# Optimization experiments

Measured on AMD Instinct MI355X. Metric: run time of the kernel, lower is better.

The kernel has to match this reference:

```python
import jax, jax.numpy as jnp
import numpy as np
import math

H, HD = 16, 64
EPS = 1e-6


def setup_inputs() -> dict:
    key = jax.random.key(0)
    ks = jax.random.split(key, 6)
    B, T, D = 4, 2048, 1024
    s = 0.02
    return {
        "x": jax.random.normal(ks[0], (B, T, D), jnp.float32),
        "wq": jax.random.normal(ks[1], (D, D), jnp.float32) * s,
        "wk": jax.random.normal(ks[2], (D, D), jnp.float32) * s,
        "wv": jax.random.normal(ks[3], (D, D), jnp.float32) * s,
        "wo": jax.random.normal(ks[4], (D, D), jnp.float32) * s,
        "norm_g": jnp.ones((D,), jnp.float32),
    }


def reference(x, wq, wk, wv, wo, norm_g):
    B, T, D = x.shape
    scale = math.sqrt(HD)
    # nn.Linear(D, D, bias=False): y = x @ W.T
    q = (x @ wq.T).reshape(B, T, H, HD).transpose(0, 2, 1, 3)  # [B,H,T,HD]
    k = (x @ wk.T).reshape(B, T, H, HD).transpose(0, 2, 1, 3)
    v = (x @ wv.T).reshape(B, T, H, HD).transpose(0, 2, 1, 3)
    scores = jnp.einsum("bhqd,bhkd->bhqk", q, k) / scale  # [B,H,T,T]
    causal = jnp.tril(jnp.ones((T, T), bool))  # True where allowed
    scores = jnp.where(causal, scores, -jnp.inf)
    attn = jax.nn.softmax(scores, axis=-1)  # dropout p=0 -> identity
    out = jnp.einsum("bhqk,bhkd->bhqd", attn, v)  # [B,H,T,HD]
    out = out.transpose(0, 2, 1, 3).reshape(B, T, D)
    y = x + out @ wo.T  # residual
    # RMSNorm
    rms = jnp.sqrt(jnp.mean(y * y, axis=-1, keepdims=True) + EPS)
    return (y / rms) * norm_g
```

## Files before the change

kernel.cpp:

```cpp
#include <hip/hip_runtime.h>
#include <hip/hip_bf16.h>

constexpr int NB  = 4;
constexpr int NT  = 2048;
constexpr int ND  = 1024;
constexpr int NH  = 16;
constexpr int NHD = 64;
constexpr int NM  = NB * NT;

typedef unsigned short u16;
typedef __attribute__((ext_vector_type(8))) short  short8;
typedef __attribute__((ext_vector_type(4))) float  f32x4;

__device__ __forceinline__ u16 f2bf(float f) {
  unsigned u = __builtin_bit_cast(unsigned, f);
  u += 0x7FFFu + ((u >> 16) & 1u);
  return (u16)(u >> 16);
}

__device__ __forceinline__ unsigned pk2bf(float lo, float hi_) {
  float2 t; t.x = lo; t.y = hi_;
  __hip_bfloat162 h2 = __float22bfloat162_rn(t);
  unsigned u;
  __builtin_memcpy(&u, &h2, 4);
  return u;
}

__device__ __forceinline__ void gll16(const u16* src, u16* dst) {
  __builtin_amdgcn_global_load_lds(
      (const __attribute__((address_space(1))) void*)src,
      (__attribute__((address_space(3))) void*)dst, 16, 0, 0);
}

__global__ __launch_bounds__(256) void cast_all(
    const float* __restrict__ x,
    const float* __restrict__ w0, const float* __restrict__ w1,
    const float* __restrict__ w2, const float* __restrict__ w3,
    u16* __restrict__ xb,
    u16* __restrict__ o0, u16* __restrict__ o1,
    u16* __restrict__ o2, u16* __restrict__ o3) {
  const int bid = blockIdx.x;
  const float* in;
  u16* out;
  int i;
  if (bid < 8192) {
    in = x; out = xb; i = bid * 256 + threadIdx.x;
  } else {
    const int z = (bid - 8192) >> 10;
    in  = (z == 0) ? w0 : (z == 1) ? w1 : (z == 2) ? w2 : w3;
    out = (z == 0) ? o0 : (z == 1) ? o1 : (z == 2) ? o2 : o3;
    i = ((bid - 8192) & 1023) * 256 + threadIdx.x;
  }
  float4 v = ((const float4*)in)[i];
  ushort4 o;
  o.x = f2bf(v.x); o.y = f2bf(v.y); o.z = f2bf(v.z); o.w = f2bf(v.w);
  ((ushort4*)out)[i] = o;
}

__global__ __launch_bounds__(512, 2) void gemm_qkvm(
    const u16* __restrict__ xb,
    const u16* __restrict__ wqb, const u16* __restrict__ wkb, const u16* __restrict__ wvb,
    u16* __restrict__ Qb, u16* __restrict__ Kb, u16* __restrict__ VTb) {
  const int row0 = blockIdx.x << 7;
  const int col0 = blockIdx.y << 7;
  const float scl = 0.125f * 1.44269504f;

  const int tid  = threadIdx.x;
  const int lane = tid & 63, wid = tid >> 6;
  const int wm = wid >> 2, wn = wid & 3;
  const int li = lane & 15, hi = lane >> 4;
  const int l3 = lane >> 3, sl = lane & 7;
  const int schunk = ((sl ^ l3) << 3);

  extern __shared__ __align__(16) u16 smem[];
  u16* lA = smem;
  u16* lB = smem + 2 * 128 * 64;

  auto stage = [&](int t) {
    const int bf = t & 1;
    const int k0 = t << 6;
#pragma unroll
    for (int h = 0; h < 2; ++h) {
      int r = h * 64 + wid * 8;
      size_t go = (size_t)(col0 + r + l3) * ND + k0 + schunk;
      gll16(&xb [(size_t)(row0 + r + l3) * ND + k0 + schunk], &lA[bf * 8192 + r * 64]);
      gll16(&wqb[go], &lB[(bf * 3 + 0) * 8192 + r * 64]);
      gll16(&wkb[go], &lB[(bf * 3 + 1) * 8192 + r * 64]);
      gll16(&wvb[go], &lB[(bf * 3 + 2) * 8192 + r * 64]);
    }
  };

  f32x4 acc[3][4][2] = {};

  stage(0);
  asm volatile("s_waitcnt vmcnt(0)" ::: "memory");
  __builtin_amdgcn_s_barrier();

  for (int i = 0; i < 16; ++i) {
    if (i + 1 < 16) stage(i + 1);

    const u16* la = &lA[(i & 1) * 8192];

    short8 a[4][2];
#pragma unroll
    for (int m = 0; m < 4; ++m)
#pragma unroll
      for (int c = 0; c < 2; ++c)
        a[m][c] = *(const short8*)&la[(wm * 64 + m * 16 + li) * 64 + (((c * 4 + hi) ^ (li & 7)) << 3)];

#pragma unroll
    for (int z = 0; z < 3; ++z) {
      const u16* lb = &lB[((i & 1) * 3 + z) * 8192];
      short8 b[2][2];
#pragma unroll
      for (int n = 0; n < 2; ++n)
#pragma unroll
        for (int c = 0; c < 2; ++c)
          b[n][c] = *(const short8*)&lb[(wn * 32 + n * 16 + li) * 64 + (((c * 4 + hi) ^ (li & 7)) << 3)];

      if (z == 2) {
#pragma unroll
        for (int m = 0; m < 4; ++m)
#pragma unroll
          for (int n = 0; n < 2; ++n)
#pragma unroll
            for (int c = 0; c < 2; ++c)
              acc[z][m][n] = __builtin_amdgcn_mfma_f32_16x16x32_bf16(a[m][c], b[n][c], acc[z][m][n], 0, 0, 0);
      } else {
#pragma unroll
        for (int m = 0; m < 4; ++m)
#pragma unroll
          for (int n = 0; n < 2; ++n)
#pragma unroll
            for (int c = 0; c < 2; ++c)
              acc[z][m][n] = __builtin_amdgcn_mfma_f32_16x16x32_bf16(b[n][c], a[m][c], acc[z][m][n], 0, 0, 0);
      }
    }

    if (i + 1 < 16) { asm volatile("s_waitcnt vmcnt(0)" ::: "memory"); }
    __builtin_amdgcn_s_barrier();
  }

#pragma unroll
  for (int m = 0; m < 4; ++m)
#pragma unroll
    for (int n = 0; n < 2; ++n) {
      {
        int token = row0 + wm * 64 + m * 16 + li;
        int feat0 = col0 + wn * 32 + n * 16 + hi * 4;
        int b_ = token >> 11, t_ = token & (NT - 1);
        int h_ = feat0 >> 6,  d0 = feat0 & (NHD - 1);
        uint2 w;
        w.x = pk2bf(acc[0][m][n][0] * scl, acc[0][m][n][1] * scl);
        w.y = pk2bf(acc[0][m][n][2] * scl, acc[0][m][n][3] * scl);
        *(uint2*)&Qb[(((size_t)(b_ * NH + h_)) * NT + t_) * NHD + d0] = w;
      }
      {
        int token = row0 + wm * 64 + m * 16 + li;
        int feat0 = col0 + wn * 32 + n * 16 + hi * 4;
        int b_ = token >> 11, t_ = token & (NT - 1);
        int h_ = feat0 >> 6,  d0 = feat0 & (NHD - 1);
        uint2 w;
        w.x = pk2bf(acc[1][m][n][0], acc[1][m][n][1]);
        w.y = pk2bf(acc[1][m][n][2], acc[1][m][n][3]);
        *(uint2*)&Kb[(((size_t)(b_ * NH + h_)) * NT + t_) * NHD + d0] = w;
      }
      {
        int token0 = row0 + wm * 64 + m * 16 + hi * 4;
        int col    = col0 + wn * 32 + n * 16 + li;
        int b_ = token0 >> 11, t0 = token0 & (NT - 1);
        int h_ = col >> 6,     d_ = col & (NHD - 1);
        uint2 w;
        w.x = pk2bf(acc[2][m][n][0], acc[2][m][n][1]);
        w.y = pk2bf(acc[2][m][n][2], acc[2][m][n][3]);
        *(uint2*)&VTb[(((size_t)(b_ * NH + h_)) * NHD + d_) * NT + t0] = w;
      }
    }
}

__global__ __launch_bounds__(512, 2) void gemm_wo3(
    const u16* __restrict__ ao, const u16* __restrict__ wob,
    const float* __restrict__ x, float* __restrict__ y) {
  const int row0 = blockIdx.x << 7;
  const int col0 = blockIdx.y << 7;

  const int tid  = threadIdx.x;
  const int lane = tid & 63, wid = tid >> 6;
  const int wm = wid >> 2, wn = wid & 3;
  const int li = lane & 15, hi = lane >> 4;
  const int l3 = lane >> 3, sl = lane & 7;
  const int schunk = ((sl ^ l3) << 3);

  extern __shared__ __align__(16) u16 smem[];
  u16* lAb = smem;
  u16* lBb = smem + 3 * 128 * 64;

  auto stage = [&](int t) {
    const int bo = (t % 3) * 8192;
    const int k0 = t << 6;
#pragma unroll
    for (int h = 0; h < 2; ++h) {
      int r = h * 64 + wid * 8;
      gll16(&ao [(size_t)(row0 + r + l3) * ND + k0 + schunk], &lAb[bo + r * 64]);
      gll16(&wob[(size_t)(col0 + r + l3) * ND + k0 + schunk], &lBb[bo + r * 64]);
    }
  };

  f32x4 acc[4][2] = {};

  stage(0);
  stage(1);

  for (int i = 0; i < 16; ++i) {
    if (i < 15) { asm volatile("s_waitcnt vmcnt(4)" ::: "memory"); }
    else        { asm volatile("s_waitcnt vmcnt(0)" ::: "memory"); }
    __builtin_amdgcn_s_barrier();

    if (i + 2 < 16) stage(i + 2);

    const u16* la = &lAb[(i % 3) * 8192];
    const u16* lb = &lBb[(i % 3) * 8192];

    short8 a[4][2], b[2][2];
#pragma unroll
    for (int m = 0; m < 4; ++m)
#pragma unroll
      for (int c = 0; c < 2; ++c)
        a[m][c] = *(const short8*)&la[(wm * 64 + m * 16 + li) * 64 + (((c * 4 + hi) ^ (li & 7)) << 3)];
#pragma unroll
    for (int n = 0; n < 2; ++n)
#pragma unroll
      for (int c = 0; c < 2; ++c)
        b[n][c] = *(const short8*)&lb[(wn * 32 + n * 16 + li) * 64 + (((c * 4 + hi) ^ (li & 7)) << 3)];

#pragma unroll
    for (int m = 0; m < 4; ++m)
#pragma unroll
      for (int n = 0; n < 2; ++n)
#pragma unroll
        for (int c = 0; c < 2; ++c)
          acc[m][n] = __builtin_amdgcn_mfma_f32_16x16x32_bf16(b[n][c], a[m][c], acc[m][n], 0, 0, 0);
  }

#pragma unroll
  for (int m = 0; m < 4; ++m)
#pragma unroll
    for (int n = 0; n < 2; ++n) {
      int token = row0 + wm * 64 + m * 16 + li;
      int feat0 = col0 + wn * 32 + n * 16 + hi * 4;
      size_t idx = (size_t)token * ND + feat0;
      float4 xv = *(const float4*)&x[idx];
      float4 o;
      o.x = acc[m][n][0] + xv.x; o.y = acc[m][n][1] + xv.y;
      o.z = acc[m][n][2] + xv.z; o.w = acc[m][n][3] + xv.w;
      *(float4*)&y[idx] = o;
    }
}

__global__ __launch_bounds__(256) void attn_kernel(
    const u16* __restrict__ Q, const u16* __restrict__ K, const u16* __restrict__ VT,
    u16* __restrict__ AO) {
  const int nb  = gridDim.x * gridDim.y;
  const int b0  = blockIdx.y * gridDim.x + blockIdx.x;
  const int L   = (b0 & 7) * (nb >> 3) + (b0 >> 3);
  const int qb  = 31 - (L & 31);
  const int bh  = L >> 5;

  const int tid = threadIdx.x;
  const int lane = tid & 63, wid = tid >> 6;
  const int li = lane & 15, hi = lane >> 4;
  const int r0 = qb * 64 + wid * 16;
  const int qrow = r0 + li;
  const size_t bK = (size_t)bh * NT * NHD;
  const size_t bV = (size_t)bh * NHD * NT;

  __shared__ __align__(16) u16 lK [2][64 * 64];
  __shared__ __align__(16) u16 lVT[3][64 * 64];
  __shared__ __align__(16) u16 lP [4][16 * 64];

  const int ch0 = tid, ch1 = tid + 256;
  const int d0 = (ch0 >> 3) * 64 + (((ch0 & 7) ^ ((ch0 >> 3) & 7)) << 3);
  const int d1 = (ch1 >> 3) * 64 + (((ch1 & 7) ^ ((ch1 >> 3) & 7)) << 3);
  const int vOff0 = (ch0 >> 3) * NT + (ch0 & 7) * 8;
  const int vOff1 = (ch1 >> 3) * NT + (ch1 & 7) * 8;

  uint4 gK0, gK1, gV0, gV1;
  auto issue = [&](int kt) {
    const u16* kp = K + bK + (size_t)kt * 4096;
    const u16* vp = VT + bV + kt * 64;
    gK0 = *(const uint4*)&kp[ch0 * 8];
    gK1 = *(const uint4*)&kp[ch1 * 8];
    gV0 = *(const uint4*)&vp[vOff0];
    gV1 = *(const uint4*)&vp[vOff1];
  };
  auto commit = [&](int kt) {
    *(uint4*)&lK [kt & 1][d0] = gK0;
    *(uint4*)&lK [kt & 1][d1] = gK1;
    *(uint4*)&lVT[kt % 3][d0] = gV0;
    *(uint4*)&lVT[kt % 3][d1] = gV1;
  };

  short8 qf[2];
#pragma unroll
  for (int c = 0; c < 2; ++c)
    qf[c] = *(const short8*)&Q[bK + (size_t)qrow * NHD + c * 32 + hi * 8];

  short8 vone;
#pragma unroll
  for (int e = 0; e < 8; ++e) vone[e] = (short)0x3F80;

  f32x4 o[4] = {};
  f32x4 o4 = {};
  short8 pap0, pap1;

  issue(0);
  commit(0);
  __syncthreads();

  const int pswz = (li & 7) << 1;

  for (int kt = 0; kt <= qb; ++kt) {
    if (kt < qb) issue(kt + 1);

    f32x4 s[4] = {};
    __builtin_amdgcn_s_setprio(1);
#pragma unroll
    for (int g = 0; g < 4; ++g)
#pragma unroll
      for (int c = 0; c < 2; ++c) {
        short8 kf = *(const short8*)&lK[kt & 1][(g * 16 + li) * 64 + ((c * 4 + hi) ^ (li & 7)) * 8];
        s[g] = __builtin_amdgcn_mfma_f32_16x16x32_bf16(kf, qf[c], s[g], 0, 0, 0);
      }

    if (kt > 0) {
      const u16* lv = lVT[(kt - 1) % 3];
#pragma unroll
      for (int gd = 0; gd < 4; ++gd) {
        short8 vf0 = *(const short8*)&lv[(gd * 16 + li) * 64 + ((0 * 4 + hi) ^ (li & 7)) * 8];
        short8 vf1 = *(const short8*)&lv[(gd * 16 + li) * 64 + ((1 * 4 + hi) ^ (li & 7)) * 8];
        o[gd] = __builtin_amdgcn_mfma_f32_16x16x32_bf16(vf0, pap0, o[gd], 0, 0, 0);
        o[gd] = __builtin_amdgcn_mfma_f32_16x16x32_bf16(vf1, pap1, o[gd], 0, 0, 0);
      }
      o4 = __builtin_amdgcn_mfma_f32_16x16x32_bf16(vone, pap0, o4, 0, 0, 0);
      o4 = __builtin_amdgcn_mfma_f32_16x16x32_bf16(vone, pap1, o4, 0, 0, 0);
    }
    __builtin_amdgcn_s_setprio(0);

    if (kt == qb) {
#pragma unroll
      for (int g = 0; g < 4; ++g)
#pragma unroll
        for (int rg = 0; rg < 4; ++rg) {
          int kcol = kt * 64 + g * 16 + hi * 4 + rg;
          if (kcol > qrow) s[g][rg] = -INFINITY;
        }
    }

#pragma unroll
    for (int g = 0; g < 4; ++g) {
      float p0 = __builtin_amdgcn_exp2f(s[g][0]);
      float p1 = __builtin_amdgcn_exp2f(s[g][1]);
      float p2 = __builtin_amdgcn_exp2f(s[g][2]);
      float p3 = __builtin_amdgcn_exp2f(s[g][3]);
      uint2 w;
      w.x = pk2bf(p0, p1);
      w.y = pk2bf(p2, p3);
      int k8s = (g * 4 + hi) ^ pswz;
      *(uint2*)&lP[wid][li * 64 + k8s * 4] = w;
    }

    pap0 = *(const short8*)&lP[wid][li * 64 + ((0 * 8 + hi * 2) ^ pswz) * 4];
    pap1 = *(const short8*)&lP[wid][li * 64 + ((1 * 8 + hi * 2) ^ pswz) * 4];

    if (kt < qb) commit(kt + 1);
    __syncthreads();
  }

  {
    const u16* lv = lVT[qb % 3];
#pragma unroll
    for (int gd = 0; gd < 4; ++gd) {
      short8 vf0 = *(const short8*)&lv[(gd * 16 + li) * 64 + ((0 * 4 + hi) ^ (li & 7)) * 8];
      short8 vf1 = *(const short8*)&lv[(gd * 16 + li) * 64 + ((1 * 4 + hi) ^ (li & 7)) * 8];
      o[gd] = __builtin_amdgcn_mfma_f32_16x16x32_bf16(vf0, pap0, o[gd], 0, 0, 0);
      o[gd] = __builtin_amdgcn_mfma_f32_16x16x32_bf16(vf1, pap1, o[gd], 0, 0, 0);
    }
    o4 = __builtin_amdgcn_mfma_f32_16x16x32_bf16(vone, pap0, o4, 0, 0, 0);
    o4 = __builtin_amdgcn_mfma_f32_16x16x32_bf16(vone, pap1, o4, 0, 0, 0);
  }

  const int b_ = bh >> 4, h_ = bh & 15;
  const float inv = 1.0f / o4[0];
  const size_t rowbase = ((size_t)(b_ * NT + qrow)) * ND + h_ * 64;
#pragma unroll
  for (int gd = 0; gd < 4; ++gd) {
    uint2 w;
    w.x = pk2bf(o[gd][0] * inv, o[gd][1] * inv);
    w.y = pk2bf(o[gd][2] * inv, o[gd][3] * inv);
    *(uint2*)&AO[rowbase + gd * 16 + hi * 4] = w;
  }
}

__global__ __launch_bounds__(256) void rmsnorm_kernel(float* __restrict__ y,
                                                      const float* __restrict__ g) {
  const int row = blockIdx.x;
  const int tid = threadIdx.x;
  const int lane = tid & 63, wid = tid >> 6;
  float4 v = ((const float4*)(y + (size_t)row * ND))[tid];
  float ss = v.x * v.x + v.y * v.y + v.z * v.z + v.w * v.w;
#pragma unroll
  for (int off = 32; off; off >>= 1) ss += __shfl_down(ss, off);
  __shared__ float red[4];
  if (lane == 0) red[wid] = ss;
  __syncthreads();
  float tot = red[0] + red[1] + red[2] + red[3];
  float inv = rsqrtf(tot * (1.0f / (float)ND) + 1e-6f);
  float4 gg = ((const float4*)g)[tid];
  float4 o;
  o.x = v.x * inv * gg.x; o.y = v.y * inv * gg.y;
  o.z = v.z * inv * gg.z; o.w = v.w * inv * gg.w;
  ((float4*)(y + (size_t)row * ND))[tid] = o;
}

extern "C" void kernel_launch(void* const* d_in, const int* in_sizes, int n_in,
                              void* d_out, int out_size, void* d_ws, size_t ws_size,
                              hipStream_t stream) {
  const float* x  = (const float*)d_in[0];
  const float* wq = (const float*)d_in[1];
  const float* wk = (const float*)d_in[2];
  const float* wv = (const float*)d_in[3];
  const float* wo = (const float*)d_in[4];
  const float* ng = (const float*)d_in[5];
  float* out = (float*)d_out;

  char* ws = (char*)d_ws;
  u16* xb  = (u16*)(ws);
  u16* wqb = (u16*)(ws + (16u << 20));
  u16* wkb = (u16*)(ws + (18u << 20));
  u16* wvb = (u16*)(ws + (20u << 20));
  u16* wob = (u16*)(ws + (22u << 20));
  u16* Qb  = (u16*)(ws + (24u << 20));
  u16* Kb  = (u16*)(ws + (40u << 20));
  u16* VTb = (u16*)(ws + (56u << 20));
  u16* AO  = (u16*)(ws + (72u << 20));

  cast_all<<<8192 + 4096, 256, 0, stream>>>(x, wq, wk, wv, wo, xb, wqb, wkb, wvb, wob);

  gemm_qkvm<<<dim3(64, 8), 512, 131072, stream>>>(xb, wqb, wkb, wvb, Qb, Kb, VTb);
  attn_kernel<<<dim3(NT / 64, NB * NH), 256, 0, stream>>>(Qb, Kb, VTb, AO);
  gemm_wo3<<<dim3(64, 8), 512, 98304, stream>>>(AO, wob, x, out);
  rmsnorm_kernel<<<NM, 256, 0, stream>>>(out, ng);
}
```

Before: 183.5 us.

## Process two KV tiles per iteration with four-deep K/V LDS buffers

Restructures the causal attention loop so each iteration loads, scores, softmaxes and accumulates two 64-wide KV tiles, with K and V staged in four LDS slots. This halves the number of block barriers and global load rounds, and removes the skewed PV-from-previous-tile pipeline in favour of in-iteration PV right after each tile's exponentials. In exchange, LDS grows from about 48KB to 72KB per block and register pressure rises, which can reduce blocks per CU. The old overlap of PV MFMAs with the next tile's QK is lost. When qb is even, the extra prefetched tile is loaded but never used.

```diff
diff --git a/kernel.cpp b/kernel.cpp
--- a/kernel.cpp
+++ b/kernel.cpp
@@ -274,8 +274,8 @@
   const size_t bK = (size_t)bh * NT * NHD;
   const size_t bV = (size_t)bh * NHD * NT;
 
-  __shared__ __align__(16) u16 lK [2][64 * 64];
-  __shared__ __align__(16) u16 lVT[3][64 * 64];
+  __shared__ __align__(16) u16 lK [4][64 * 64];
+  __shared__ __align__(16) u16 lVT[4][64 * 64];
   __shared__ __align__(16) u16 lP [4][16 * 64];
 
   const int ch0 = tid, ch1 = tid + 256;
@@ -284,20 +284,32 @@
   const int vOff0 = (ch0 >> 3) * NT + (ch0 & 7) * 8;
   const int vOff1 = (ch1 >> 3) * NT + (ch1 & 7) * 8;
 
-  uint4 gK0, gK1, gV0, gV1;
-  auto issue = [&](int kt) {
-    const u16* kp = K + bK + (size_t)kt * 4096;
-    const u16* vp = VT + bV + kt * 64;
-    gK0 = *(const uint4*)&kp[ch0 * 8];
-    gK1 = *(const uint4*)&kp[ch1 * 8];
-    gV0 = *(const uint4*)&vp[vOff0];
-    gV1 = *(const uint4*)&vp[vOff1];
+  uint4 gKa0, gKa1, gVa0, gVa1;
+  uint4 gKb0, gKb1, gVb0, gVb1;
+  auto issue = [&](int j) {
+    const u16* kpa = K + bK + (size_t)(2 * j) * 4096;
+    const u16* vpa = VT + bV + (size_t)(2 * j) * 64;
+    gKa0 = *(const uint4*)&kpa[ch0 * 8];
+    gKa1 = *(const uint4*)&kpa[ch1 * 8];
+    gVa0 = *(const uint4*)&vpa[vOff0];
+    gVa1 = *(const uint4*)&vpa[vOff1];
+    const u16* kpb = kpa + 4096;
+    const u16* vpb = vpa + 64;
+    gKb0 = *(const uint4*)&kpb[ch0 * 8];
+    gKb1 = *(const uint4*)&kpb[ch1 * 8];
+    gVb0 = *(const uint4*)&vpb[vOff0];
+    gVb1 = *(const uint4*)&vpb[vOff1];
   };
-  auto commit = [&](int kt) {
-    *(uint4*)&lK [kt & 1][d0] = gK0;
-    *(uint4*)&lK [kt & 1][d1] = gK1;
-    *(uint4*)&lVT[kt % 3][d0] = gV0;
-    *(uint4*)&lVT[kt % 3][d1] = gV1;
+  auto commit = [&](int j) {
+    const int ba = (2 * j) & 3, bb = (2 * j + 1) & 3;
+    *(uint4*)&lK [ba][d0] = gKa0;
+    *(uint4*)&lK [ba][d1] = gKa1;
+    *(uint4*)&lVT[ba][d0] = gVa0;
+    *(uint4*)&lVT[ba][d1] = gVa1;
+    *(uint4*)&lK [bb][d0] = gKb0;
+    *(uint4*)&lK [bb][d1] = gKb1;
+    *(uint4*)&lVT[bb][d0] = gVb0;
+    *(uint4*)&lVT[bb][d1] = gVb1;
   };
 
   short8 qf[2];
@@ -311,82 +323,121 @@
 
   f32x4 o[4] = {};
   f32x4 o4 = {};
-  short8 pap0, pap1;
 
   issue(0);
   commit(0);
   __syncthreads();
 
+  const int jmax = qb >> 1;
   const int pswz = (li & 7) << 1;
 
-  for (int kt = 0; kt <= qb; ++kt) {
-    if (kt < qb) issue(kt + 1);
-
-    f32x4 s[4] = {};
+  for (int j = 0; j <= jmax; ++j) {
+    if (j < jmax) issue(j + 1);
+
+    const int s0t = 2 * j, s1t = 2 * j + 1;
+    const bool act1 = (s1t <= qb);
+
+    f32x4 sA[4] = {}, sB[4] = {};
     __builtin_amdgcn_s_setprio(1);
 #pragma unroll
     for (int g = 0; g < 4; ++g)
 #pragma unroll
       for (int c = 0; c < 2; ++c) {
-        short8 kf = *(const short8*)&lK[kt & 1][(g * 16 + li) * 64 + ((c * 4 + hi) ^ (li & 7)) * 8];
-        s[g] = __builtin_amdgcn_mfma_f32_16x16x32_bf16(kf, qf[c], s[g], 0, 0, 0);
-      }
-
-    if (kt > 0) {
-      const u16* lv = lVT[(kt - 1) % 3];
+        short8 kf = *(const short8*)&lK[s0t & 3][(g * 16 + li) * 64 + ((c * 4 + hi) ^ (li & 7)) * 8];
+        sA[g] = __builtin_amdgcn_mfma_f32_16x16x32_bf16(kf, qf[c], sA[g], 0, 0, 0);
+      }
+    if (act1) {
+#pragma unroll
+      for (int g = 0; g < 4; ++g)
+#pragma unroll
+        for (int c = 0; c < 2; ++c) {
+          short8 kf = *(const short8*)&lK[s1t & 3][(g * 16 + li) * 64 + ((c * 4 + hi) ^ (li & 7)) * 8];
+          sB[g] = __builtin_amdgcn_mfma_f32_16x16x32_bf16(kf, qf[c], sB[g], 0, 0, 0);
+        }
+    }
+    __builtin_amdgcn_s_setprio(0);
+
+    if (s0t == qb) {
+#pragma unroll
+      for (int g = 0; g < 4; ++g)
+#pragma unroll
+        for (int rg = 0; rg < 4; ++rg) {
+          int kcol = s0t * 64 + g * 16 + hi * 4 + rg;
+          if (kcol > qrow) sA[g][rg] = -INFINITY;
+        }
+    }
+    if (act1 && s1t == qb) {
+#pragma unroll
+      for (int g = 0; g < 4; ++g)
+#pragma unroll
+        for (int rg = 0; rg < 4; ++rg) {
+          int kcol = s1t * 64 + g * 16 + hi * 4 + rg;
+          if (kcol > qrow) sB[g][rg] = -INFINITY;
+        }
+    }
+
+    {
+#pragma unroll
+      for (int g = 0; g < 4; ++g) {
+        float p0 = __builtin_amdgcn_exp2f(sA[g][0]);
+        float p1 = __builtin_amdgcn_exp2f(sA[g][1]);
+        float p2 = __builtin_amdgcn_exp2f(sA[g][2]);
+        float p3 = __builtin_amdgcn_exp2f(sA[g][3]);
+        uint2 w;
+        w.x = pk2bf(p0, p1);
+        w.y = pk2bf(p2, p3);
+        int k8s = (g * 4 + hi) ^ pswz;
+        *(uint2*)&lP[wid][li * 64 + k8s * 4] = w;
+      }
+      short8 pa0 = *(const short8*)&lP[wid][li * 64 + ((0 * 8 + hi * 2) ^ pswz) * 4];
+      short8 pa1 = *(const short8*)&lP[wid][li * 64 + ((1 * 8 + hi * 2) ^ pswz) * 4];
+
+      const u16* lv = lVT[s0t & 3];
+      __builtin_amdgcn_s_setprio(1);
 #pragma unroll
       for (int gd = 0; gd < 4; ++gd) {
         short8 vf0 = *(const short8*)&lv[(gd * 16 + li) * 64 + ((0 * 4 + hi) ^ (li & 7)) * 8];
         short8 vf1 = *(const short8*)&lv[(gd * 16 + li) * 64 + ((1 * 4 + hi) ^ (li & 7)) * 8];
-        o[gd] = __builtin_amdgcn_mfma_f32_16x16x32_bf16(vf0, pap0, o[gd], 0, 0, 0);
-        o[gd] = __builtin_amdgcn_mfma_f32_16x16x32_bf16(vf1, pap1, o[gd], 0, 0, 0);
-      }
-      o4 = __builtin_amdgcn_mfma_f32_16x16x32_bf16(vone, pap0, o4, 0, 0, 0);
-      o4 = __builtin_amdgcn_mfma_f32_16x16x32_bf16(vone, pap1, o4, 0, 0, 0);
-    }
-    __builtin_amdgcn_s_setprio(0);
-
-    if (kt == qb) {
-#pragma unroll
-      for (int g = 0; g < 4; ++g)
-#pragma unroll
-        for (int rg = 0; rg < 4; ++rg) {
-          int kcol = kt * 64 + g * 16 + hi * 4 + rg;
-          if (kcol > qrow) s[g][rg] = -INFINITY;
-        }
-    }
-
-#pragma unroll
-    for (int g = 0; g < 4; ++g) {
-      float p0 = __builtin_amdgcn_exp2f(s[g][0]);
-      float p1 = __builtin_amdgcn_exp2f(s[g][1]);
-      float p2 = __builtin_amdgcn_exp2f(s[g][2]);
-      float p3 = __builtin_amdgcn_exp2f(s[g][3]);
-      uint2 w;
-      w.x = pk2bf(p0, p1);
-      w.y = pk2bf(p2, p3);
-      int k8s = (g * 4 + hi) ^ pswz;
-      *(uint2*)&lP[wid][li * 64 + k8s * 4] = w;
-    }
-
-    pap0 = *(const short8*)&lP[wid][li * 64 + ((0 * 8 + hi * 2) ^ pswz) * 4];
-    pap1 = *(const short8*)&lP[wid][li * 64 + ((1 * 8 + hi * 2) ^ pswz) * 4];
-
-    if (kt < qb) commit(kt + 1);
+        o[gd] = __builtin_amdgcn_mfma_f32_16x16x32_bf16(vf0, pa0, o[gd], 0, 0, 0);
+        o[gd] = __builtin_amdgcn_mfma_f32_16x16x32_bf16(vf1, pa1, o[gd], 0, 0, 0);
+      }
+      o4 = __builtin_amdgcn_mfma_f32_16x16x32_bf16(vone, pa0, o4, 0, 0, 0);
+      o4 = __builtin_amdgcn_mfma_f32_16x16x32_bf16(vone, pa1, o4, 0, 0, 0);
+      __builtin_amdgcn_s_setprio(0);
+    }
+
+    if (act1) {
+#pragma unroll
+      for (int g = 0; g < 4; ++g) {
+        float p0 = __builtin_amdgcn_exp2f(sB[g][0]);
+        float p1 = __builtin_amdgcn_exp2f(sB[g][1]);
+        float p2 = __builtin_amdgcn_exp2f(sB[g][2]);
+        float p3 = __builtin_amdgcn_exp2f(sB[g][3]);
+        uint2 w;
+        w.x = pk2bf(p0, p1);
+        w.y = pk2bf(p2, p3);
+        int k8s = (g * 4 + hi) ^ pswz;
+        *(uint2*)&lP[wid][li * 64 + k8s * 4] = w;
+      }
+      short8 pb0 = *(const short8*)&lP[wid][li * 64 + ((0 * 8 + hi * 2) ^ pswz) * 4];
+      short8 pb1 = *(const short8*)&lP[wid][li * 64 + ((1 * 8 + hi * 2) ^ pswz) * 4];
+
+      const u16* lv = lVT[s1t & 3];
+      __builtin_amdgcn_s_setprio(1);
+#pragma unroll
+      for (int gd = 0; gd < 4; ++gd) {
+        short8 vf0 = *(const short8*)&lv[(gd * 16 + li) * 64 + ((0 * 4 + hi) ^ (li & 7)) * 8];
+        short8 vf1 = *(const short8*)&lv[(gd * 16 + li) * 64 + ((1 * 4 + hi) ^ (li & 7)) * 8];
+        o[gd] = __builtin_amdgcn_mfma_f32_16x16x32_bf16(vf0, pb0, o[gd], 0, 0, 0);
+        o[gd] = __builtin_amdgcn_mfma_f32_16x16x32_bf16(vf1, pb1, o[gd], 0, 0, 0);
+      }
+      o4 = __builtin_amdgcn_mfma_f32_16x16x32_bf16(vone, pb0, o4, 0, 0, 0);
+      o4 = __builtin_amdgcn_mfma_f32_16x16x32_bf16(vone, pb1, o4, 0, 0, 0);
+      __builtin_amdgcn_s_setprio(0);
+    }
+
+    if (j < jmax) commit(j + 1);
     __syncthreads();
-  }
-
-  {
-    const u16* lv = lVT[qb % 3];
-#pragma unroll
-    for (int gd = 0; gd < 4; ++gd) {
-      short8 vf0 = *(const short8*)&lv[(gd * 16 + li) * 64 + ((0 * 4 + hi) ^ (li & 7)) * 8];
-      short8 vf1 = *(const short8*)&lv[(gd * 16 + li) * 64 + ((1 * 4 + hi) ^ (li & 7)) * 8];
-      o[gd] = __builtin_amdgcn_mfma_f32_16x16x32_bf16(vf0, pap0, o[gd], 0, 0, 0);
-      o[gd] = __builtin_amdgcn_mfma_f32_16x16x32_bf16(vf1, pap1, o[gd], 0, 0, 0);
-    }
-    o4 = __builtin_amdgcn_mfma_f32_16x16x32_bf16(vone, pap0, o4, 0, 0, 0);
-    o4 = __builtin_amdgcn_mfma_f32_16x16x32_bf16(vone, pap1, o4, 0, 0, 0);
   }
 
   const int b_ = bh >> 4, h_ = bh & 15;
```

Measured after the change: 199.9 us. 9.0% more time.
